# Kernel optimization log

Measured on AMD Instinct MI355X. Metric: run time of the kernel, lower is better.

Reference implementation:

```python
import jax, jax.numpy as jnp
import numpy as np

N = 50000
E = 800000
EPS = 1e-5


def layer_norm(h, g, b):
    m = jnp.mean(h, axis=-1, keepdims=True)
    v = jnp.mean((h - m) ** 2, axis=-1, keepdims=True)
    return (h - m) * jax.lax.rsqrt(v + EPS) * g + b


def gcn_conv(x, src, dst, w, W, b):
    # PyG GCNConv: add self-loops (weight 1), symmetric normalization,
    # linear transform, scatter-add aggregation at dst, plus bias.
    n = x.shape[0]
    loop = jnp.arange(n)
    s = jnp.concatenate([src, loop])
    d = jnp.concatenate([dst, loop])
    wf = jnp.concatenate([w, jnp.ones((n,), dtype=x.dtype)])
    deg = jax.ops.segment_sum(wf, d, num_segments=n)
    dinv = jnp.where(deg > 0, deg, 1.0) ** -0.5
    dinv = jnp.where(deg > 0, dinv, 0.0)
    norm = dinv[s] * wf * dinv[d]            # [E+N]
    h = x @ W                                 # [N, out]
    msg = h[s] * norm[:, None]                # gather + scale
    out = jax.ops.segment_sum(msg, d, num_segments=n)  # scatter-add
    return out + b


def setup_inputs() -> dict:
    key = jax.random.key(0)
    ks = jax.random.split(key, 16)
    din, dh, dout = 128, 128, 64
    p = lambda k, shp: jax.random.normal(k, shp, dtype=jnp.float32) * 0.05
    return {
        "x": jax.random.normal(ks[0], (N, din), dtype=jnp.float32),
        "edge_index": jax.random.randint(ks[1], (2, E), 0, N),
        "edge_weight": jax.random.uniform(ks[2], (E,), dtype=jnp.float32),
        "W1": p(ks[3], (din, dh)), "b1": jnp.zeros((dh,), jnp.float32),
        "g1": jnp.ones((dh,), jnp.float32), "t1": jnp.zeros((dh,), jnp.float32),
        "W2": p(ks[4], (dh, dh)), "b2": jnp.zeros((dh,), jnp.float32),
        "g2": jnp.ones((dh,), jnp.float32), "t2": jnp.zeros((dh,), jnp.float32),
        "W3": p(ks[5], (dh, dout)), "b3": jnp.zeros((dout,), jnp.float32),
        "g3": jnp.ones((dout,), jnp.float32), "t3": jnp.zeros((dout,), jnp.float32),
    }


def reference(x, edge_index, edge_weight, W1, b1, g1, t1, W2, b2, g2, t2, W3, b3, g3, t3):
    src, dst = edge_index[0], edge_index[1]
    h = gcn_conv(x, src, dst, edge_weight, W1, b1)
    h = jax.nn.relu(layer_norm(h, g1, t1))
    h = gcn_conv(h, src, dst, edge_weight, W2, b2)
    h = jax.nn.relu(layer_norm(h, g2, t2))
    h = gcn_conv(h, src, dst, edge_weight, W3, b3)
    h = layer_norm(h, g3, t3)  # last layer: no relu/dropout
    return h
```

## Files before the change

kernel.cpp:

```cpp
#include <hip/hip_runtime.h>


typedef __attribute__((ext_vector_type(8))) short short8;
typedef __attribute__((ext_vector_type(4))) float f32x4;

static constexpr float FXS  = 16777216.0f;
static constexpr float FXSI = 1.0f / 16777216.0f;

__device__ __forceinline__ unsigned short f2bf(float f) {
    unsigned int u = __float_as_uint(f);
    u += 0x7FFFu + ((u >> 16) & 1u);
    return (unsigned short)(u >> 16);
}
__device__ __forceinline__ float bflo(unsigned int w) { return __uint_as_float(w << 16); }
__device__ __forceinline__ float bfhi(unsigned int w) { return __uint_as_float(w & 0xFFFF0000u); }

__global__ __launch_bounds__(256) void prep_kernel(
    const int* __restrict__ dst, const float* __restrict__ ew,
    unsigned long long* __restrict__ packed, int* __restrict__ rank, int nE, int eb,
    const float* __restrict__ X, unsigned short* __restrict__ Xb, int total4, int xbk,
    const float* __restrict__ W1, const float* __restrict__ W2,
    const float* __restrict__ W3, unsigned short* __restrict__ Wt1,
    unsigned short* __restrict__ Wt2, unsigned short* __restrict__ Wt3)
{
    const int b = blockIdx.x;
    if (b < eb) {
        const int e = b * 256 + threadIdx.x;
        if (e < nE) {
            const int d = dst[e];
            const unsigned long long fx = (unsigned long long)__float2uint_rn(ew[e] * FXS);
            const unsigned long long old = atomicAdd(&packed[d], (1ULL << 40) | fx);
            rank[e] = (int)(old >> 40);
        }
    } else if (b < eb + xbk) {
        const int i = (b - eb) * 256 + threadIdx.x;
        if (i < total4) {
            const float4 v = ((const float4*)X)[i];
            ushort4 o;
            o.x = f2bf(v.x); o.y = f2bf(v.y); o.z = f2bf(v.z); o.w = f2bf(v.w);
            ((ushort4*)Xb)[i] = o;
        }
    } else {
        const int i = (b - eb - xbk) * 256 + threadIdx.x;
        if (i < 16384) {
            const int j = i >> 7, k = i & 127;
            Wt1[i] = f2bf(W1[k * 128 + j]);
        } else if (i < 32768) {
            const int q = i - 16384, j = q >> 7, k = q & 127;
            Wt2[q] = f2bf(W2[k * 128 + j]);
        } else if (i < 40960) {
            const int q = i - 32768, j = q >> 7, k = q & 127;
            Wt3[q] = f2bf(W3[k * 64 + j]);
        }
    }
}

__global__ __launch_bounds__(256) void dinv_partial_kernel(
    const unsigned long long* __restrict__ packed, int* __restrict__ partials,
    float* __restrict__ dinv, int n)
{
    const int b = blockIdx.x;
    const int i = b * 256 + threadIdx.x;
    int c = 0;
    if (i < n) {
        const unsigned long long p = packed[i];
        c = (int)(p >> 40);
        const float deg = (float)(p & ((1ULL << 40) - 1)) * FXSI;
        dinv[i] = rsqrtf(deg + 1.0f);
    }
#pragma unroll
    for (int off = 32; off; off >>= 1) c += __shfl_xor(c, off);
    __shared__ int red[4];
    if ((threadIdx.x & 63) == 0) red[threadIdx.x >> 6] = c;
    __syncthreads();
    if (threadIdx.x == 0) partials[b] = red[0] + red[1] + red[2] + red[3];
}

__global__ __launch_bounds__(256) void scanp_kernel(
    int* __restrict__ partials, int* __restrict__ rowptr, int n, int nblk)
{
    __shared__ int buf[256];
    const int v = (threadIdx.x < nblk) ? partials[threadIdx.x] : 0;
    buf[threadIdx.x] = v;
    __syncthreads();
    for (int off = 1; off < 256; off <<= 1) {
        const int t = (threadIdx.x >= off) ? buf[threadIdx.x - off] : 0;
        __syncthreads();
        buf[threadIdx.x] += t;
        __syncthreads();
    }
    if (threadIdx.x < nblk) partials[threadIdx.x] = buf[threadIdx.x] - v;
    if (threadIdx.x == 255) rowptr[n] = buf[255];
}

__global__ __launch_bounds__(256) void scanf_kernel(
    const unsigned long long* __restrict__ packed, const int* __restrict__ partials,
    int* __restrict__ rowptr, int n)
{
    __shared__ int buf[256];
    const int b = blockIdx.x;
    const int i = b * 256 + threadIdx.x;
    const int v = (i < n) ? (int)(packed[i] >> 40) : 0;
    buf[threadIdx.x] = v;
    __syncthreads();
    for (int off = 1; off < 256; off <<= 1) {
        const int t = (threadIdx.x >= off) ? buf[threadIdx.x - off] : 0;
        __syncthreads();
        buf[threadIdx.x] += t;
        __syncthreads();
    }
    if (i < n) rowptr[i] = buf[threadIdx.x] - v + partials[b];
}

__global__ __launch_bounds__(256) void fill2_kernel(
    const int* __restrict__ src, const int* __restrict__ dst,
    const float* __restrict__ ew, const int* __restrict__ rank,
    const float* __restrict__ dinv, const int* __restrict__ rowptr,
    int2* __restrict__ edges, int nE)
{
    int e = blockIdx.x * 256 + threadIdx.x;
    if (e >= nE) return;
    const int s = src[e], d = dst[e];
    const float nrm = dinv[s] * ew[e] * dinv[d];
    edges[rowptr[d] + rank[e]] = make_int2(s, __float_as_int(nrm));
}

template<int DOUT>
__global__ __launch_bounds__(256) void gemm_mfma_kernel(
    const unsigned short* __restrict__ Xb,
    const unsigned short* __restrict__ Wt,
    unsigned short* __restrict__ H, int n)
{
    const int wave = threadIdx.x >> 6;
    const int lane = threadIdx.x & 63;
    const int row0 = (blockIdx.x * 4 + wave) * 16;
    if (row0 >= n) return;
    const int lr = lane & 15;
    const int lk = (lane >> 4) * 8;

    constexpr int NCT = DOUT / 16;
    f32x4 acc[NCT];
#pragma unroll
    for (int c = 0; c < NCT; ++c) acc[c] = (f32x4){0.f, 0.f, 0.f, 0.f};

    const int arow = row0 + lr;
    const bool rv = arow < n;
    short8 afrag[4];
#pragma unroll
    for (int ks = 0; ks < 4; ++ks)
        afrag[ks] = rv ? *(const short8*)(Xb + (size_t)arow * 128 + ks * 32 + lk)
                       : (short8){0, 0, 0, 0, 0, 0, 0, 0};

#pragma unroll
    for (int c = 0; c < NCT; ++c) {
        const unsigned short* wp = Wt + (size_t)(c * 16 + lr) * 128 + lk;
#pragma unroll
        for (int ks = 0; ks < 4; ++ks) {
            const short8 bfrag = *(const short8*)(wp + ks * 32);
            acc[c] = __builtin_amdgcn_mfma_f32_16x16x32_bf16(afrag[ks], bfrag, acc[c], 0, 0, 0);
        }
    }

    const int orow0 = row0 + (lane >> 4) * 4;
#pragma unroll
    for (int c = 0; c < NCT; ++c) {
#pragma unroll
        for (int r = 0; r < 4; ++r) {
            const int orow = orow0 + r;
            if (orow < n) H[(size_t)orow * DOUT + c * 16 + lr] = f2bf(acc[c][r]);
        }
    }
}

template<int D, bool RELU, bool OB16>
__global__ __launch_bounds__(256) void gather_ln_kernel(
    const unsigned short* __restrict__ H, const int2* __restrict__ edges,
    const int* __restrict__ rowptr, const float* __restrict__ dinv,
    const float* __restrict__ bias, const float* __restrict__ g,
    const float* __restrict__ t, void* __restrict__ OUT, int n)
{
    constexpr int GS  = D / 8;
    constexpr int NPW = 64 / GS;
    const int lane = threadIdx.x & 63;
    const int wave = threadIdx.x >> 6;
    const int L    = lane & (GS - 1);
    const int gb0  = lane & ~(GS - 1);
    const int node = (blockIdx.x * 4 + wave) * NPW + (lane >> (GS == 16 ? 4 : 3));
    if (node >= n) return;

    const float di = dinv[node];
    const float sn = di * di;
    float acc[8];
    {
        const uint4 w = *(const uint4*)(H + (size_t)node * D + L * 8);
        const float4 b0 = *(const float4*)(bias + L * 8);
        const float4 b1 = *(const float4*)(bias + L * 8 + 4);
        acc[0] = fmaf(bflo(w.x), sn, b0.x); acc[1] = fmaf(bfhi(w.x), sn, b0.y);
        acc[2] = fmaf(bflo(w.y), sn, b0.z); acc[3] = fmaf(bfhi(w.y), sn, b0.w);
        acc[4] = fmaf(bflo(w.z), sn, b1.x); acc[5] = fmaf(bfhi(w.z), sn, b1.y);
        acc[6] = fmaf(bflo(w.w), sn, b1.z); acc[7] = fmaf(bfhi(w.w), sn, b1.w);
    }

    const int k0 = rowptr[node], k1 = rowptr[node + 1];
    for (int base = k0; base < k1; base += GS) {
        int2 ed = make_int2(0, 0);
        if (base + L < k1) ed = edges[base + L];
        const int cnt = min(GS, k1 - base);
        int j = 0;
        for (; j + 2 <= cnt; j += 2) {
            const int   s0 = __shfl(ed.x, gb0 + j);
            const int   s1 = __shfl(ed.x, gb0 + j + 1);
            const float n0 = __int_as_float(__shfl(ed.y, gb0 + j));
            const float n1 = __int_as_float(__shfl(ed.y, gb0 + j + 1));
            const uint4 w0 = *(const uint4*)(H + (size_t)s0 * D + L * 8);
            const uint4 w1 = *(const uint4*)(H + (size_t)s1 * D + L * 8);
            acc[0] = fmaf(bflo(w0.x), n0, acc[0]); acc[1] = fmaf(bfhi(w0.x), n0, acc[1]);
            acc[2] = fmaf(bflo(w0.y), n0, acc[2]); acc[3] = fmaf(bfhi(w0.y), n0, acc[3]);
            acc[4] = fmaf(bflo(w0.z), n0, acc[4]); acc[5] = fmaf(bfhi(w0.z), n0, acc[5]);
            acc[6] = fmaf(bflo(w0.w), n0, acc[6]); acc[7] = fmaf(bfhi(w0.w), n0, acc[7]);
            acc[0] = fmaf(bflo(w1.x), n1, acc[0]); acc[1] = fmaf(bfhi(w1.x), n1, acc[1]);
            acc[2] = fmaf(bflo(w1.y), n1, acc[2]); acc[3] = fmaf(bfhi(w1.y), n1, acc[3]);
            acc[4] = fmaf(bflo(w1.z), n1, acc[4]); acc[5] = fmaf(bfhi(w1.z), n1, acc[5]);
            acc[6] = fmaf(bflo(w1.w), n1, acc[6]); acc[7] = fmaf(bfhi(w1.w), n1, acc[7]);
        }
        if (j < cnt) {
            const int   s0 = __shfl(ed.x, gb0 + j);
            const float n0 = __int_as_float(__shfl(ed.y, gb0 + j));
            const uint4 w0 = *(const uint4*)(H + (size_t)s0 * D + L * 8);
            acc[0] = fmaf(bflo(w0.x), n0, acc[0]); acc[1] = fmaf(bfhi(w0.x), n0, acc[1]);
            acc[2] = fmaf(bflo(w0.y), n0, acc[2]); acc[3] = fmaf(bfhi(w0.y), n0, acc[3]);
            acc[4] = fmaf(bflo(w0.z), n0, acc[4]); acc[5] = fmaf(bfhi(w0.z), n0, acc[5]);
            acc[6] = fmaf(bflo(w0.w), n0, acc[6]); acc[7] = fmaf(bfhi(w0.w), n0, acc[7]);
        }
    }

    float s1 = 0.f;
#pragma unroll
    for (int i = 0; i < 8; ++i) s1 += acc[i];
#pragma unroll
    for (int off = GS / 2; off; off >>= 1) s1 += __shfl_xor(s1, off);
    const float m = s1 * (1.f / D);
    float s2 = 0.f;
#pragma unroll
    for (int i = 0; i < 8; ++i) { acc[i] -= m; s2 += acc[i] * acc[i]; }
#pragma unroll
    for (int off = GS / 2; off; off >>= 1) s2 += __shfl_xor(s2, off);
    const float rs = rsqrtf(s2 * (1.f / D) + 1e-5f);

    const float4 g0 = *(const float4*)(g + L * 8), g1 = *(const float4*)(g + L * 8 + 4);
    const float4 t0 = *(const float4*)(t + L * 8), t1 = *(const float4*)(t + L * 8 + 4);
    float r[8];
    r[0] = fmaf(acc[0] * rs, g0.x, t0.x); r[1] = fmaf(acc[1] * rs, g0.y, t0.y);
    r[2] = fmaf(acc[2] * rs, g0.z, t0.z); r[3] = fmaf(acc[3] * rs, g0.w, t0.w);
    r[4] = fmaf(acc[4] * rs, g1.x, t1.x); r[5] = fmaf(acc[5] * rs, g1.y, t1.y);
    r[6] = fmaf(acc[6] * rs, g1.z, t1.z); r[7] = fmaf(acc[7] * rs, g1.w, t1.w);
    if (RELU) {
#pragma unroll
        for (int i = 0; i < 8; ++i) r[i] = fmaxf(r[i], 0.f);
    }

    if constexpr (OB16) {
        uint4 o;
        o.x = (unsigned int)f2bf(r[0]) | ((unsigned int)f2bf(r[1]) << 16);
        o.y = (unsigned int)f2bf(r[2]) | ((unsigned int)f2bf(r[3]) << 16);
        o.z = (unsigned int)f2bf(r[4]) | ((unsigned int)f2bf(r[5]) << 16);
        o.w = (unsigned int)f2bf(r[6]) | ((unsigned int)f2bf(r[7]) << 16);
        *(uint4*)((unsigned short*)OUT + (size_t)node * D + L * 8) = o;
    } else {
        float* o = (float*)OUT + (size_t)node * D + L * 8;
        *(float4*)o       = make_float4(r[0], r[1], r[2], r[3]);
        *(float4*)(o + 4) = make_float4(r[4], r[5], r[6], r[7]);
    }
}

extern "C" void kernel_launch(void* const* d_in, const int* in_sizes, int n_in,
                              void* d_out, int out_size, void* d_ws, size_t ws_size,
                              hipStream_t stream)
{
    const float* x  = (const float*)d_in[0];
    const int*   ei = (const int*)  d_in[1];
    const float* ew = (const float*)d_in[2];
    const float* W1 = (const float*)d_in[3];
    const float* b1 = (const float*)d_in[4];
    const float* g1 = (const float*)d_in[5];
    const float* t1 = (const float*)d_in[6];
    const float* W2 = (const float*)d_in[7];
    const float* b2 = (const float*)d_in[8];
    const float* g2 = (const float*)d_in[9];
    const float* t2 = (const float*)d_in[10];
    const float* W3 = (const float*)d_in[11];
    const float* b3 = (const float*)d_in[12];
    const float* g3 = (const float*)d_in[13];
    const float* t3 = (const float*)d_in[14];

    const int n  = in_sizes[0] / 128;
    const int nE = in_sizes[1] / 2;
    const int* srcv = ei;
    const int* dstv = ei + nE;

    const size_t na   = ((size_t)n + 63) & ~(size_t)63;
    const int    nblk = (n + 255) / 256;
    const int    eb   = (nE + 255) / 256;
    const int    xbk  = (n * 32 + 255) / 256;

    unsigned long long* packed = (unsigned long long*)d_ws;
    float* dinv     = (float*)(packed + na);
    int*   rowptr   = (int*)(dinv + na);
    int*   partials = rowptr + na + 64;
    int2*  edges    = (int2*)(partials + 256);
    unsigned short* Hb  = (unsigned short*)(edges + nE);
    unsigned short* Qb  = Hb + (size_t)n * 128;
    unsigned short* xb  = Qb + (size_t)n * 128;
    unsigned short* Wt1 = xb + (size_t)n * 128;
    unsigned short* Wt2 = Wt1 + 16384;
    unsigned short* Wt3 = Wt2 + 16384;
    int* rank = (int*)Hb;

    hipMemsetAsync(packed, 0, na * sizeof(unsigned long long), stream);

    prep_kernel<<<eb + xbk + 160, 256, 0, stream>>>(
        dstv, ew, packed, rank, nE, eb,
        x, xb, n * 32, xbk, W1, W2, W3, Wt1, Wt2, Wt3);
    dinv_partial_kernel<<<nblk, 256, 0, stream>>>(packed, partials, dinv, n);
    scanp_kernel       <<<1,    256, 0, stream>>>(partials, rowptr, n, nblk);
    scanf_kernel       <<<nblk, 256, 0, stream>>>(packed, partials, rowptr, n);
    fill2_kernel       <<<eb,   256, 0, stream>>>(srcv, dstv, ew, rank, dinv, rowptr, edges, nE);

    const int gb   = (n + 63) / 64;
    const int nbA  = (n + 15) / 16;
    const int nbB  = (n + 31) / 32;

    gemm_mfma_kernel<128><<<gb, 256, 0, stream>>>(xb, Wt1, Hb, n);
    gather_ln_kernel<128, true, true><<<nbA, 256, 0, stream>>>(Hb, edges, rowptr, dinv, b1, g1, t1, Qb, n);

    gemm_mfma_kernel<128><<<gb, 256, 0, stream>>>(Qb, Wt2, Hb, n);
    gather_ln_kernel<128, true, true><<<nbA, 256, 0, stream>>>(Hb, edges, rowptr, dinv, b2, g2, t2, Qb, n);

    gemm_mfma_kernel<64><<<gb, 256, 0, stream>>>(Qb, Wt3, Hb, n);
    gather_ln_kernel<64, false, false><<<nbB, 256, 0, stream>>>(Hb, edges, rowptr, dinv, b3, g3, t3, d_out, n);
}
```

Before: 302.0 us.

## Fuse CSR fill with first GEMM and batch edge atomics and gathers

Merges the edge fill kernel and the first-layer GEMM into one launch whose blocks are split by index, so the two independent jobs overlap and one launch is saved. The rank scratch moves from Hb to Qb so the GEMM can write Hb while fill reads rank. Prep now handles four edges per thread to keep more atomics in flight, fill handles two edges per thread, and the gather loop is unrolled to four edges with all loads issued before the FMAs. This raises register pressure and makes the block mix uneven within the fused launch.

```diff
diff --git a/kernel.cpp b/kernel.cpp
--- a/kernel.cpp
+++ b/kernel.cpp
@@ -15,25 +15,44 @@
 __device__ __forceinline__ float bflo(unsigned int w) { return __uint_as_float(w << 16); }
 __device__ __forceinline__ float bfhi(unsigned int w) { return __uint_as_float(w & 0xFFFF0000u); }
 
+__device__ __forceinline__ void accum8(float* acc, const uint4 w, float nr) {
+    acc[0] = fmaf(bflo(w.x), nr, acc[0]); acc[1] = fmaf(bfhi(w.x), nr, acc[1]);
+    acc[2] = fmaf(bflo(w.y), nr, acc[2]); acc[3] = fmaf(bfhi(w.y), nr, acc[3]);
+    acc[4] = fmaf(bflo(w.z), nr, acc[4]); acc[5] = fmaf(bfhi(w.z), nr, acc[5]);
+    acc[6] = fmaf(bflo(w.w), nr, acc[6]); acc[7] = fmaf(bfhi(w.w), nr, acc[7]);
+}
+
 __global__ __launch_bounds__(256) void prep_kernel(
     const int* __restrict__ dst, const float* __restrict__ ew,
-    unsigned long long* __restrict__ packed, int* __restrict__ rank, int nE, int eb,
+    unsigned long long* __restrict__ packed, int* __restrict__ rank, int nE, int eb4,
     const float* __restrict__ X, unsigned short* __restrict__ Xb, int total4, int xbk,
     const float* __restrict__ W1, const float* __restrict__ W2,
     const float* __restrict__ W3, unsigned short* __restrict__ Wt1,
     unsigned short* __restrict__ Wt2, unsigned short* __restrict__ Wt3)
 {
     const int b = blockIdx.x;
-    if (b < eb) {
-        const int e = b * 256 + threadIdx.x;
-        if (e < nE) {
-            const int d = dst[e];
-            const unsigned long long fx = (unsigned long long)__float2uint_rn(ew[e] * FXS);
-            const unsigned long long old = atomicAdd(&packed[d], (1ULL << 40) | fx);
-            rank[e] = (int)(old >> 40);
-        }
-    } else if (b < eb + xbk) {
-        const int i = (b - eb) * 256 + threadIdx.x;
+    if (b < eb4) {
+        const int e0 = b * 1024 + threadIdx.x;
+        int   d[4]; float w[4]; bool v[4];
+#pragma unroll
+        for (int u = 0; u < 4; ++u) {
+            const int e = e0 + u * 256;
+            v[u] = e < nE;
+            if (v[u]) { d[u] = dst[e]; w[u] = ew[e]; }
+        }
+        unsigned long long old[4];
+#pragma unroll
+        for (int u = 0; u < 4; ++u)
+            if (v[u]) {
+                const unsigned long long fx =
+                    (unsigned long long)__float2uint_rn(w[u] * FXS);
+                old[u] = atomicAdd(&packed[d[u]], (1ULL << 40) | fx);
+            }
+#pragma unroll
+        for (int u = 0; u < 4; ++u)
+            if (v[u]) rank[e0 + u * 256] = (int)(old[u] >> 40);
+    } else if (b < eb4 + xbk) {
+        const int i = (b - eb4) * 256 + threadIdx.x;
         if (i < total4) {
             const float4 v = ((const float4*)X)[i];
             ushort4 o;
@@ -41,7 +60,7 @@
             ((ushort4*)Xb)[i] = o;
         }
     } else {
-        const int i = (b - eb - xbk) * 256 + threadIdx.x;
+        const int i = (b - eb4 - xbk) * 256 + threadIdx.x;
         if (i < 16384) {
             const int j = i >> 7, k = i & 127;
             Wt1[i] = f2bf(W1[k * 128 + j]);
@@ -112,28 +131,33 @@
     if (i < n) rowptr[i] = buf[threadIdx.x] - v + partials[b];
 }
 
-__global__ __launch_bounds__(256) void fill2_kernel(
+__device__ __forceinline__ void fill_body(
     const int* __restrict__ src, const int* __restrict__ dst,
     const float* __restrict__ ew, const int* __restrict__ rank,
     const float* __restrict__ dinv, const int* __restrict__ rowptr,
-    int2* __restrict__ edges, int nE)
-{
-    int e = blockIdx.x * 256 + threadIdx.x;
-    if (e >= nE) return;
-    const int s = src[e], d = dst[e];
-    const float nrm = dinv[s] * ew[e] * dinv[d];
-    edges[rowptr[d] + rank[e]] = make_int2(s, __float_as_int(nrm));
+    int2* __restrict__ edges, int nE, int bid, int tid)
+{
+    const int e0 = bid * 512 + tid;
+#pragma unroll
+    for (int u = 0; u < 2; ++u) {
+        const int e = e0 + u * 256;
+        if (e < nE) {
+            const int s = src[e], d = dst[e];
+            const float nrm = dinv[s] * ew[e] * dinv[d];
+            edges[rowptr[d] + rank[e]] = make_int2(s, __float_as_int(nrm));
+        }
+    }
 }
 
 template<int DOUT>
-__global__ __launch_bounds__(256) void gemm_mfma_kernel(
+__device__ __forceinline__ void gemm_body(
     const unsigned short* __restrict__ Xb,
     const unsigned short* __restrict__ Wt,
-    unsigned short* __restrict__ H, int n)
-{
-    const int wave = threadIdx.x >> 6;
-    const int lane = threadIdx.x & 63;
-    const int row0 = (blockIdx.x * 4 + wave) * 16;
+    unsigned short* __restrict__ H, int n, int bid, int tid)
+{
+    const int wave = tid >> 6;
+    const int lane = tid & 63;
+    const int row0 = (bid * 4 + wave) * 16;
     if (row0 >= n) return;
     const int lr = lane & 15;
     const int lk = (lane >> 4) * 8;
@@ -170,6 +194,28 @@
             if (orow < n) H[(size_t)orow * DOUT + c * 16 + lr] = f2bf(acc[c][r]);
         }
     }
+}
+
+__global__ __launch_bounds__(256) void fill_gemm1_kernel(
+    const int* __restrict__ src, const int* __restrict__ dst,
+    const float* __restrict__ ew, const int* __restrict__ rank,
+    const float* __restrict__ dinv, const int* __restrict__ rowptr,
+    int2* __restrict__ edges, int nE, int fb,
+    const unsigned short* __restrict__ Xb, const unsigned short* __restrict__ Wt,
+    unsigned short* __restrict__ H, int n)
+{
+    if ((int)blockIdx.x < fb)
+        fill_body(src, dst, ew, rank, dinv, rowptr, edges, nE, blockIdx.x, threadIdx.x);
+    else
+        gemm_body<128>(Xb, Wt, H, n, blockIdx.x - fb, threadIdx.x);
+}
+
+template<int DOUT>
+__global__ __launch_bounds__(256) void gemm_mfma_kernel(
+    const unsigned short* __restrict__ Xb, const unsigned short* __restrict__ Wt,
+    unsigned short* __restrict__ H, int n)
+{
+    gemm_body<DOUT>(Xb, Wt, H, n, blockIdx.x, threadIdx.x);
 }
 
 template<int D, bool RELU, bool OB16>
@@ -207,30 +253,24 @@
         if (base + L < k1) ed = edges[base + L];
         const int cnt = min(GS, k1 - base);
         int j = 0;
-        for (; j + 2 <= cnt; j += 2) {
-            const int   s0 = __shfl(ed.x, gb0 + j);
-            const int   s1 = __shfl(ed.x, gb0 + j + 1);
-            const float n0 = __int_as_float(__shfl(ed.y, gb0 + j));
-            const float n1 = __int_as_float(__shfl(ed.y, gb0 + j + 1));
-            const uint4 w0 = *(const uint4*)(H + (size_t)s0 * D + L * 8);
-            const uint4 w1 = *(const uint4*)(H + (size_t)s1 * D + L * 8);
-            acc[0] = fmaf(bflo(w0.x), n0, acc[0]); acc[1] = fmaf(bfhi(w0.x), n0, acc[1]);
-            acc[2] = fmaf(bflo(w0.y), n0, acc[2]); acc[3] = fmaf(bfhi(w0.y), n0, acc[3]);
-            acc[4] = fmaf(bflo(w0.z), n0, acc[4]); acc[5] = fmaf(bfhi(w0.z), n0, acc[5]);
-            acc[6] = fmaf(bflo(w0.w), n0, acc[6]); acc[7] = fmaf(bfhi(w0.w), n0, acc[7]);
-            acc[0] = fmaf(bflo(w1.x), n1, acc[0]); acc[1] = fmaf(bfhi(w1.x), n1, acc[1]);
-            acc[2] = fmaf(bflo(w1.y), n1, acc[2]); acc[3] = fmaf(bfhi(w1.y), n1, acc[3]);
-            acc[4] = fmaf(bflo(w1.z), n1, acc[4]); acc[5] = fmaf(bfhi(w1.z), n1, acc[5]);
-            acc[6] = fmaf(bflo(w1.w), n1, acc[6]); acc[7] = fmaf(bfhi(w1.w), n1, acc[7]);
-        }
-        if (j < cnt) {
+        for (; j + 4 <= cnt; j += 4) {
+            int s[4]; float nr[4]; uint4 w[4];
+#pragma unroll
+            for (int u = 0; u < 4; ++u) {
+                s[u]  = __shfl(ed.x, gb0 + j + u);
+                nr[u] = __int_as_float(__shfl(ed.y, gb0 + j + u));
+            }
+#pragma unroll
+            for (int u = 0; u < 4; ++u)
+                w[u] = *(const uint4*)(H + (size_t)s[u] * D + L * 8);
+#pragma unroll
+            for (int u = 0; u < 4; ++u) accum8(acc, w[u], nr[u]);
+        }
+        for (; j < cnt; ++j) {
             const int   s0 = __shfl(ed.x, gb0 + j);
             const float n0 = __int_as_float(__shfl(ed.y, gb0 + j));
             const uint4 w0 = *(const uint4*)(H + (size_t)s0 * D + L * 8);
-            acc[0] = fmaf(bflo(w0.x), n0, acc[0]); acc[1] = fmaf(bfhi(w0.x), n0, acc[1]);
-            acc[2] = fmaf(bflo(w0.y), n0, acc[2]); acc[3] = fmaf(bfhi(w0.y), n0, acc[3]);
-            acc[4] = fmaf(bflo(w0.z), n0, acc[4]); acc[5] = fmaf(bfhi(w0.z), n0, acc[5]);
-            acc[6] = fmaf(bflo(w0.w), n0, acc[6]); acc[7] = fmaf(bfhi(w0.w), n0, acc[7]);
+            accum8(acc, w0, n0);
         }
     }
 
@@ -300,8 +340,9 @@
 
     const size_t na   = ((size_t)n + 63) & ~(size_t)63;
     const int    nblk = (n + 255) / 256;
-    const int    eb   = (nE + 255) / 256;
+    const int    eb4  = (nE + 1023) / 1024;
     const int    xbk  = (n * 32 + 255) / 256;
+    const int    fb   = (nE + 511) / 512;
 
     unsigned long long* packed = (unsigned long long*)d_ws;
     float* dinv     = (float*)(packed + na);
@@ -314,23 +355,23 @@
     unsigned short* Wt1 = xb + (size_t)n * 128;
     unsigned short* Wt2 = Wt1 + 16384;
     unsigned short* Wt3 = Wt2 + 16384;
-    int* rank = (int*)Hb;
+    int* rank = (int*)Qb;
 
     hipMemsetAsync(packed, 0, na * sizeof(unsigned long long), stream);
 
-    prep_kernel<<<eb + xbk + 160, 256, 0, stream>>>(
-        dstv, ew, packed, rank, nE, eb,
+    prep_kernel<<<eb4 + xbk + 160, 256, 0, stream>>>(
+        dstv, ew, packed, rank, nE, eb4,
         x, xb, n * 32, xbk, W1, W2, W3, Wt1, Wt2, Wt3);
     dinv_partial_kernel<<<nblk, 256, 0, stream>>>(packed, partials, dinv, n);
     scanp_kernel       <<<1,    256, 0, stream>>>(partials, rowptr, n, nblk);
     scanf_kernel       <<<nblk, 256, 0, stream>>>(packed, partials, rowptr, n);
-    fill2_kernel       <<<eb,   256, 0, stream>>>(srcv, dstv, ew, rank, dinv, rowptr, edges, nE);
 
     const int gb   = (n + 63) / 64;
     const int nbA  = (n + 15) / 16;
     const int nbB  = (n + 31) / 32;
 
-    gemm_mfma_kernel<128><<<gb, 256, 0, stream>>>(xb, Wt1, Hb, n);
+    fill_gemm1_kernel<<<fb + gb, 256, 0, stream>>>(
+        srcv, dstv, ew, rank, dinv, rowptr, edges, nE, fb, xb, Wt1, Hb, n);
     gather_ln_kernel<128, true, true><<<nbA, 256, 0, stream>>>(Hb, edges, rowptr, dinv, b1, g1, t1, Qb, n);
 
     gemm_mfma_kernel<128><<<gb, 256, 0, stream>>>(Qb, Wt2, Hb, n);
```

Result: no change. 298.8 us (-1.1%).
